# Kernel tuning notes

Hardware: AMD Instinct MI355X
Metric: run time of the kernel (lower is better)

The kernel has to match this reference:

```python
import jax, jax.numpy as jnp
import numpy as np

# GCN ('gcn' variant): avg-pooled adjacency, per-step linear + propagation + ReLU,
# final output projection, then select the target (first) node of each block.
# The original builds a dense block-diagonal (B*n, B*n) adjacency via torch.block_diag;
# since off-block entries are exactly zero, this is mathematically identical to
# batched per-block matmuls, which is what we do here.

B, N_NODES, D_IN, D_HID, D_OUT, STEPS = 256, 512, 256, 256, 128, 3


def setup_inputs() -> dict:
    key = jax.random.key(0)
    ks = jax.random.split(key, 6)
    xavier = lambda k, shp: jax.random.normal(k, shp, jnp.float32) * np.sqrt(2.0 / (shp[0] + shp[1]))
    feat = jax.random.normal(ks[0], (B * N_NODES, D_IN), jnp.float32)
    raw_adj = jax.random.uniform(ks[1], (B, N_NODES, N_NODES), jnp.float32)
    W0 = xavier(ks[2], (D_IN, D_HID))
    W1 = xavier(ks[3], (D_HID, D_HID))
    W2 = xavier(ks[4], (D_HID, D_HID))
    Wout = xavier(ks[5], (D_HID, D_OUT))
    return {"feat": feat, "raw_adj": raw_adj, "W0": W0, "W1": W1, "W2": W2, "Wout": Wout}


def reference(feat, raw_adj, W0, W1, W2, Wout):
    b, n, _ = raw_adj.shape
    d = feat.shape[1]
    Xb = feat.reshape(b, n, d)  # block view of feat

    # avg_pooling: row-normalize adjacency by the sum over columns whose
    # feature rows are nonzero (block-diagonal => per-block computation).
    nz = (jnp.linalg.norm(Xb, axis=2) > 0).astype(raw_adj.dtype)  # (b, n)
    row_sum = jnp.einsum('bij,bj->bi', raw_adj, nz)               # (b, n)
    row_sum = jnp.where(row_sum == 0, 1.0, row_sum)
    adj = raw_adj / row_sum[:, :, None]

    X = Xb
    for W in (W0, W1, W2):
        Z = jnp.einsum('bnd,dh->bnh', X, W)      # per-step linear (no bias)
        X = jax.nn.relu(jnp.einsum('bij,bjh->bih', adj, Z))  # propagate + ReLU
    out = jnp.einsum('bnh,ho->bno', X, Wout)     # output layer
    # X[ids] with ids = [0, n, 2n, ...] == first node of each block
    return out[:, 0, :]
```

## Files before the change

kernel.cpp:

```cpp
#include <hip/hip_runtime.h>


typedef __attribute__((ext_vector_type(8))) short short8;
typedef __attribute__((ext_vector_type(4))) float f32x4;

__device__ __forceinline__ unsigned short f2bf(float x) {
  unsigned u = __float_as_uint(x);
  unsigned r = u + 0x7fffu + ((u >> 16) & 1u);
  return (unsigned short)(r >> 16);
}
__device__ __forceinline__ float bf2f(unsigned short b) {
  return __uint_as_float(((unsigned)b) << 16);
}
__device__ __forceinline__ unsigned pkbf(float lo, float hi) {
  unsigned r;
  asm("v_cvt_pk_bf16_f32 %0, %1, %2" : "=v"(r) : "v"(lo), "v"(hi));
  return r;
}

#define GLDS(g, l) __builtin_amdgcn_global_load_lds( \
    (const __attribute__((address_space(1))) void*)(g), \
    (__attribute__((address_space(3))) void*)(l), 16, 0, 0)

__device__ __forceinline__ int swz2048(int bid) { return (bid & 7) * 256 + (bid >> 3); }

__global__ void k_wconv(const float* __restrict__ W0, const float* __restrict__ W1,
                        unsigned short* __restrict__ Wt) {
  int s = blockIdx.x >> 8;
  int n = blockIdx.x & 255;
  int k = threadIdx.x;
  const float* W = s ? W1 : W0;
  Wt[(size_t)s * 65536 + n * 256 + k] = f2bf(W[(size_t)k * 256 + n]);
}

__global__ void k_adj(const float* __restrict__ adj, const float* __restrict__ nz,
                      unsigned short* __restrict__ adjN) {
  int row = blockIdx.x * 4 + (threadIdx.x >> 6);
  int lane = threadIdx.x & 63;
  int b = row >> 9;
  const float4* src = (const float4*)(adj + (size_t)row * 512);
  float4 a0 = src[lane * 2], a1 = src[lane * 2 + 1];
  const float4* nzp = (const float4*)(nz + (size_t)b * 512);
  float4 z0 = nzp[lane * 2], z1 = nzp[lane * 2 + 1];
  float s = a0.x * z0.x + a0.y * z0.y + a0.z * z0.z + a0.w * z0.w
          + a1.x * z1.x + a1.y * z1.y + a1.z * z1.z + a1.w * z1.w;
#pragma unroll
  for (int off = 1; off < 64; off <<= 1) s += __shfl_xor(s, off);
  float inv = 1.f / ((s == 0.f) ? 1.f : s);
  uint4 p;
  p.x = pkbf(a0.x * inv, a0.y * inv);
  p.y = pkbf(a0.z * inv, a0.w * inv);
  p.z = pkbf(a1.x * inv, a1.y * inv);
  p.w = pkbf(a1.z * inv, a1.w * inv);
  ((uint4*)(adjN + (size_t)row * 512))[lane] = p;
}

__device__ __forceinline__ void gemm_tile(
    const char* Ag, int ldaB, const char* Bg, int ldbB, int nkt,
    char* ldsA, char* ldsB, f32x4 acc[4][4], int wm, int wn, int lane, int tid) {
  for (int kt = 0; kt < nkt; ++kt) {
#pragma unroll
    for (int q = 0; q < 4; ++q) {
      int P = (q * 256 + tid) * 16;
      int L = P ^ (((P >> 7) & 7) << 4);
      int row = L >> 7, cb = L & 127;
      GLDS(Ag + (size_t)row * ldaB + kt * 128 + cb, ldsA + P);
      GLDS(Bg + (size_t)row * ldbB + kt * 128 + cb, ldsB + P);
    }
    __syncthreads();
#pragma unroll
    for (int ks = 0; ks < 2; ++ks) {
      short8 af[4], bfr[4];
      int c = ks * 64 + ((lane >> 4) << 4);
#pragma unroll
      for (int m = 0; m < 4; ++m) {
        int row = wm * 64 + m * 16 + (lane & 15);
        af[m] = *(const short8*)(ldsA + ((row * 128 + c) ^ ((row & 7) << 4)));
      }
#pragma unroll
      for (int n = 0; n < 4; ++n) {
        int row = wn * 64 + n * 16 + (lane & 15);
        bfr[n] = *(const short8*)(ldsB + ((row * 128 + c) ^ ((row & 7) << 4)));
      }
#pragma unroll
      for (int m = 0; m < 4; ++m)
#pragma unroll
        for (int n = 0; n < 4; ++n)
          acc[m][n] = __builtin_amdgcn_mfma_f32_16x16x32_bf16(af[m], bfr[n], acc[m][n], 0, 0, 0);
    }
    __syncthreads();
  }
}

__global__ __launch_bounds__(256) void k_lin0(const float* __restrict__ feat,
                                              const unsigned short* __restrict__ Wt,
                                              unsigned short* __restrict__ Zt,
                                              float* __restrict__ nzOut) {
  __shared__ char ldsA[16384];
  __shared__ char ldsB[16384];
  int tid = threadIdx.x, lane = tid & 63, wid = tid >> 6;
  int wm = wid >> 1, wn = wid & 1;
  int tile = swz2048(blockIdx.x);
  int tm = tile >> 1, tn = tile & 1;
  const float* Ag = feat + (size_t)tm * 128 * 256;
  const char* Bg = (const char*)(Wt + (size_t)tn * 128 * 256);
  int r = tid >> 1, hk = tid & 1;
  const float* myrow = Ag + (size_t)r * 256 + hk * 32;
  float ssq = 0.f;
  f32x4 acc[4][4];
#pragma unroll
  for (int m = 0; m < 4; ++m)
#pragma unroll
    for (int n = 0; n < 4; ++n) { f32x4 z = {0.f, 0.f, 0.f, 0.f}; acc[m][n] = z; }

  for (int kt = 0; kt < 4; ++kt) {
#pragma unroll
    for (int q = 0; q < 4; ++q) {
      int P = (q * 256 + tid) * 16;
      int L = P ^ (((P >> 7) & 7) << 4);
      int row = L >> 7, cb = L & 127;
      GLDS(Bg + (size_t)row * 512 + kt * 128 + cb, ldsB + P);
    }
    float4 f[8];
#pragma unroll
    for (int q = 0; q < 8; ++q) f[q] = ((const float4*)(myrow + kt * 64))[q];
#pragma unroll
    for (int q = 0; q < 8; ++q)
      ssq += f[q].x * f[q].x + f[q].y * f[q].y + f[q].z * f[q].z + f[q].w * f[q].w;
#pragma unroll
    for (int q = 0; q < 4; ++q) {
      uint4 w;
      w.x = pkbf(f[2 * q].x, f[2 * q].y);
      w.y = pkbf(f[2 * q].z, f[2 * q].w);
      w.z = pkbf(f[2 * q + 1].x, f[2 * q + 1].y);
      w.w = pkbf(f[2 * q + 1].z, f[2 * q + 1].w);
      int cb = hk * 64 + q * 16;
      *(uint4*)(ldsA + ((r * 128 + cb) ^ ((r & 7) << 4))) = w;
    }
    __syncthreads();
#pragma unroll
    for (int ks = 0; ks < 2; ++ks) {
      short8 af[4], bfr[4];
      int c = ks * 64 + ((lane >> 4) << 4);
#pragma unroll
      for (int m = 0; m < 4; ++m) {
        int row = wm * 64 + m * 16 + (lane & 15);
        af[m] = *(const short8*)(ldsA + ((row * 128 + c) ^ ((row & 7) << 4)));
      }
#pragma unroll
      for (int n = 0; n < 4; ++n) {
        int row = wn * 64 + n * 16 + (lane & 15);
        bfr[n] = *(const short8*)(ldsB + ((row * 128 + c) ^ ((row & 7) << 4)));
      }
#pragma unroll
      for (int m = 0; m < 4; ++m)
#pragma unroll
        for (int n = 0; n < 4; ++n)
          acc[m][n] = __builtin_amdgcn_mfma_f32_16x16x32_bf16(af[m], bfr[n], acc[m][n], 0, 0, 0);
    }
    __syncthreads();
  }

  float tot = ssq + __shfl_xor(ssq, 1);
  if (hk == 0 && tn == 0) nzOut[(size_t)tm * 128 + r] = (tot > 0.f) ? 1.f : 0.f;

  int b = tm >> 2;
  int node_base = ((tm & 3) * 128) + wm * 64;
  int h_base = tn * 128 + wn * 64;
#pragma unroll
  for (int m = 0; m < 4; ++m) {
    int node = node_base + m * 16 + ((lane >> 4) << 2);
#pragma unroll
    for (int n = 0; n < 4; ++n) {
      int h = h_base + n * 16 + (lane & 15);
      f32x4 v = acc[m][n];
      ushort4 p;
      p.x = f2bf(v[0]); p.y = f2bf(v[1]); p.z = f2bf(v[2]); p.w = f2bf(v[3]);
      *(ushort4*)(Zt + ((size_t)b * 256 + h) * 512 + node) = p;
    }
  }
}

__global__ __launch_bounds__(256) void k_prop(const unsigned short* __restrict__ adjN,
                                              const unsigned short* __restrict__ Zt,
                                              unsigned short* __restrict__ Xout) {
  __shared__ char lds[32768];
  int tid = threadIdx.x, lane = tid & 63, wid = tid >> 6;
  int wm = wid >> 1, wn = wid & 1;
  int tile = swz2048(blockIdx.x);
  int b = tile >> 3, tm = (tile >> 1) & 3, tn = tile & 1;
  const char* Ag = (const char*)(adjN + ((size_t)b * 512 + tm * 128) * 512);
  const char* Bg = (const char*)(Zt + ((size_t)b * 256 + tn * 128) * 512);
  f32x4 acc[4][4];
#pragma unroll
  for (int m = 0; m < 4; ++m)
#pragma unroll
    for (int n = 0; n < 4; ++n) { f32x4 z = {0.f, 0.f, 0.f, 0.f}; acc[m][n] = z; }
  gemm_tile(Ag, 1024, Bg, 1024, 8, lds, lds + 16384, acc, wm, wn, lane, tid);
  int node_base = tm * 128 + wm * 64;
  int h_base = tn * 128 + wn * 64;
#pragma unroll
  for (int m = 0; m < 4; ++m) {
    int node = node_base + m * 16 + ((lane >> 4) << 2);
#pragma unroll
    for (int n = 0; n < 4; ++n) {
      int h = h_base + n * 16 + (lane & 15);
#pragma unroll
      for (int r = 0; r < 4; ++r) {
        float v = acc[m][n][r];
        v = v > 0.f ? v : 0.f;
        Xout[((size_t)b * 512 + node + r) * 256 + h] = f2bf(v);
      }
    }
  }
}

__global__ __launch_bounds__(256) void k_linear(const unsigned short* __restrict__ X,
                                                const unsigned short* __restrict__ Wt,
                                                unsigned short* __restrict__ Zt) {
  __shared__ char lds[32768];
  int tid = threadIdx.x, lane = tid & 63, wid = tid >> 6;
  int wm = wid >> 1, wn = wid & 1;
  int tile = swz2048(blockIdx.x);
  int tm = tile >> 1, tn = tile & 1;
  const char* Ag = (const char*)(X + (size_t)tm * 128 * 256);
  const char* Bg = (const char*)(Wt + (size_t)tn * 128 * 256);
  f32x4 acc[4][4];
#pragma unroll
  for (int m = 0; m < 4; ++m)
#pragma unroll
    for (int n = 0; n < 4; ++n) { f32x4 z = {0.f, 0.f, 0.f, 0.f}; acc[m][n] = z; }
  gemm_tile(Ag, 512, Bg, 512, 4, lds, lds + 16384, acc, wm, wn, lane, tid);
  int b = tm >> 2;
  int node_base = ((tm & 3) * 128) + wm * 64;
  int h_base = tn * 128 + wn * 64;
#pragma unroll
  for (int m = 0; m < 4; ++m) {
    int node = node_base + m * 16 + ((lane >> 4) << 2);
#pragma unroll
    for (int n = 0; n < 4; ++n) {
      int h = h_base + n * 16 + (lane & 15);
      f32x4 v = acc[m][n];
      ushort4 p;
      p.x = f2bf(v[0]); p.y = f2bf(v[1]); p.z = f2bf(v[2]); p.w = f2bf(v[3]);
      *(ushort4*)(Zt + ((size_t)b * 256 + h) * 512 + node) = p;
    }
  }
}

__global__ __launch_bounds__(256) void k_tail(const unsigned short* __restrict__ adjN,
                                              const unsigned short* __restrict__ X2,
                                              const float* __restrict__ W2,
                                              const float* __restrict__ Wout,
                                              float* __restrict__ out) {
  __shared__ float aL[512];
  __shared__ float yL[8][256];
  __shared__ float y[256];
  __shared__ float x3[256];
  int b = blockIdx.x, tid = threadIdx.x;
  {
    const unsigned short* a0 = adjN + (size_t)b * 512 * 512;
    ushort2 v = ((const ushort2*)a0)[tid];
    aL[tid * 2] = bf2f(v.x);
    aL[tid * 2 + 1] = bf2f(v.y);
  }
  __syncthreads();
  {
    int hg = tid & 31, jg = tid >> 5;
    float acc8[8] = {0.f, 0.f, 0.f, 0.f, 0.f, 0.f, 0.f, 0.f};
    const unsigned short* Xb = X2 + (size_t)b * 512 * 256;
    for (int jj = 0; jj < 64; ++jj) {
      int j = jj * 8 + jg;
      short8 xv = *(const short8*)(Xb + (size_t)j * 256 + hg * 8);
      float a = aL[j];
#pragma unroll
      for (int r = 0; r < 8; ++r) acc8[r] += a * bf2f((unsigned short)xv[r]);
    }
#pragma unroll
    for (int r = 0; r < 8; ++r) yL[jg][hg * 8 + r] = acc8[r];
  }
  __syncthreads();
  {
    float s = 0.f;
#pragma unroll
    for (int g = 0; g < 8; ++g) s += yL[g][tid];
    y[tid] = s;
  }
  __syncthreads();
  {
    float s = 0.f;
    for (int k = 0; k < 256; ++k) s += y[k] * W2[(size_t)k * 256 + tid];
    x3[tid] = s > 0.f ? s : 0.f;
  }
  __syncthreads();
  if (tid < 128) {
    float s = 0.f;
    for (int h = 0; h < 256; ++h) s += x3[h] * Wout[(size_t)h * 128 + tid];
    out[(size_t)b * 128 + tid] = s;
  }
}

extern "C" void kernel_launch(void* const* d_in, const int* in_sizes, int n_in,
                              void* d_out, int out_size, void* d_ws, size_t ws_size,
                              hipStream_t stream) {
  (void)in_sizes; (void)n_in; (void)out_size; (void)ws_size;
  const float* feat = (const float*)d_in[0];
  const float* adj  = (const float*)d_in[1];
  const float* W0   = (const float*)d_in[2];
  const float* W1   = (const float*)d_in[3];
  const float* W2   = (const float*)d_in[4];
  const float* Wout = (const float*)d_in[5];
  float* out = (float*)d_out;

  char* ws = (char*)d_ws;
  unsigned short* adjN = (unsigned short*)(ws);
  unsigned short* Xbuf = (unsigned short*)(ws + 134217728);
  unsigned short* Zt   = (unsigned short*)(ws + 201326592);
  float* nzbuf         = (float*)(ws + 268435456);
  unsigned short* Wt   = (unsigned short*)(ws + 268959744);

  k_wconv<<<512, 256, 0, stream>>>(W0, W1, Wt);
  k_lin0<<<2048, 256, 0, stream>>>(feat, Wt, Zt, nzbuf);
  k_adj<<<32768, 256, 0, stream>>>(adj, nzbuf, adjN);
  k_prop<<<2048, 256, 0, stream>>>(adjN, Zt, Xbuf);
  k_linear<<<2048, 256, 0, stream>>>(Xbuf, Wt + 65536, Zt);
  k_prop<<<2048, 256, 0, stream>>>(adjN, Zt, Xbuf);
  k_tail<<<256, 256, 0, stream>>>(adjN, Xbuf, W2, Wout, out);
}
```

Before: 342.2 us.

## Double-buffer GEMM LDS staging and fuse the last propagation with row-0 reduction

The shared GEMM tile loop now double-buffers its LDS stages, so the global-to-LDS loads for the next K tile are issued while MFMAs run on the current one. The second propagation kernel no longer writes the full X2 activation. It applies ReLU and immediately reduces against row 0 of the adjacency to produce partial y vectors, which the tail kernel then sums. This removes a full X2 write and re-read plus the tail's gather pass. In exchange, LDS per block doubles to 64KB, which may lower occupancy.

```diff
diff --git a/kernel.cpp b/kernel.cpp
--- a/kernel.cpp
+++ b/kernel.cpp
@@ -55,19 +55,27 @@
   ((uint4*)(adjN + (size_t)row * 512))[lane] = p;
 }
 
-__device__ __forceinline__ void gemm_tile(
+__device__ __forceinline__ void gemm_dbuf(
     const char* Ag, int ldaB, const char* Bg, int ldbB, int nkt,
-    char* ldsA, char* ldsB, f32x4 acc[4][4], int wm, int wn, int lane, int tid) {
+    char* lds, f32x4 acc[4][4], int wm, int wn, int lane, int tid) {
+  char* ldsA = lds;
+  char* ldsB = lds + 32768;
+#define STAGE_AB(KT, BUF) do {                                           \
+    _Pragma("unroll")                                                    \
+    for (int q = 0; q < 4; ++q) {                                        \
+      int P = (q * 256 + tid) * 16;                                      \
+      int L = P ^ (((P >> 7) & 7) << 4);                                 \
+      int row = L >> 7, cb = L & 127;                                    \
+      GLDS(Ag + (size_t)row * ldaB + (KT) * 128 + cb,                    \
+           ldsA + (BUF) * 16384 + P);                                    \
+      GLDS(Bg + (size_t)row * ldbB + (KT) * 128 + cb,                    \
+           ldsB + (BUF) * 16384 + P);                                    \
+    } } while (0)
+  STAGE_AB(0, 0);
+  __syncthreads();
   for (int kt = 0; kt < nkt; ++kt) {
-#pragma unroll
-    for (int q = 0; q < 4; ++q) {
-      int P = (q * 256 + tid) * 16;
-      int L = P ^ (((P >> 7) & 7) << 4);
-      int row = L >> 7, cb = L & 127;
-      GLDS(Ag + (size_t)row * ldaB + kt * 128 + cb, ldsA + P);
-      GLDS(Bg + (size_t)row * ldbB + kt * 128 + cb, ldsB + P);
-    }
-    __syncthreads();
+    int cur = kt & 1;
+    if (kt + 1 < nkt) STAGE_AB(kt + 1, cur ^ 1);
 #pragma unroll
     for (int ks = 0; ks < 2; ++ks) {
       short8 af[4], bfr[4];
@@ -75,12 +83,12 @@
 #pragma unroll
       for (int m = 0; m < 4; ++m) {
         int row = wm * 64 + m * 16 + (lane & 15);
-        af[m] = *(const short8*)(ldsA + ((row * 128 + c) ^ ((row & 7) << 4)));
+        af[m] = *(const short8*)(ldsA + cur * 16384 + ((row * 128 + c) ^ ((row & 7) << 4)));
       }
 #pragma unroll
       for (int n = 0; n < 4; ++n) {
         int row = wn * 64 + n * 16 + (lane & 15);
-        bfr[n] = *(const short8*)(ldsB + ((row * 128 + c) ^ ((row & 7) << 4)));
+        bfr[n] = *(const short8*)(ldsB + cur * 16384 + ((row * 128 + c) ^ ((row & 7) << 4)));
       }
 #pragma unroll
       for (int m = 0; m < 4; ++m)
@@ -90,6 +98,7 @@
     }
     __syncthreads();
   }
+#undef STAGE_AB
 }
 
 __global__ __launch_bounds__(256) void k_lin0(const float* __restrict__ feat,
@@ -184,7 +193,7 @@
 __global__ __launch_bounds__(256) void k_prop(const unsigned short* __restrict__ adjN,
                                               const unsigned short* __restrict__ Zt,
                                               unsigned short* __restrict__ Xout) {
-  __shared__ char lds[32768];
+  __shared__ char lds[65536];
   int tid = threadIdx.x, lane = tid & 63, wid = tid >> 6;
   int wm = wid >> 1, wn = wid & 1;
   int tile = swz2048(blockIdx.x);
@@ -196,7 +205,7 @@
   for (int m = 0; m < 4; ++m)
 #pragma unroll
     for (int n = 0; n < 4; ++n) { f32x4 z = {0.f, 0.f, 0.f, 0.f}; acc[m][n] = z; }
-  gemm_tile(Ag, 1024, Bg, 1024, 8, lds, lds + 16384, acc, wm, wn, lane, tid);
+  gemm_dbuf(Ag, 1024, Bg, 1024, 8, lds, acc, wm, wn, lane, tid);
   int node_base = tm * 128 + wm * 64;
   int h_base = tn * 128 + wn * 64;
 #pragma unroll
@@ -215,10 +224,58 @@
   }
 }
 
+__global__ __launch_bounds__(256) void k_propy(const unsigned short* __restrict__ adjN,
+                                               const unsigned short* __restrict__ Zt,
+                                               float* __restrict__ yws) {
+  __shared__ char lds[65536];
+  __shared__ float ybuf[2][128];
+  int tid = threadIdx.x, lane = tid & 63, wid = tid >> 6;
+  int wm = wid >> 1, wn = wid & 1;
+  int tile = swz2048(blockIdx.x);
+  int b = tile >> 3, tm = (tile >> 1) & 3, tn = tile & 1;
+  const char* Ag = (const char*)(adjN + ((size_t)b * 512 + tm * 128) * 512);
+  const char* Bg = (const char*)(Zt + ((size_t)b * 256 + tn * 128) * 512);
+  f32x4 acc[4][4];
+#pragma unroll
+  for (int m = 0; m < 4; ++m)
+#pragma unroll
+    for (int n = 0; n < 4; ++n) { f32x4 z = {0.f, 0.f, 0.f, 0.f}; acc[m][n] = z; }
+  gemm_dbuf(Ag, 1024, Bg, 1024, 8, lds, acc, wm, wn, lane, tid);
+
+  int kq = lane >> 4, r0 = lane & 15;
+  float yp[4] = {0.f, 0.f, 0.f, 0.f};
+#pragma unroll
+  for (int m = 0; m < 4; ++m) {
+    int node = tm * 128 + wm * 64 + m * 16 + kq * 4;
+    ushort4 a4 = *(const ushort4*)(adjN + (size_t)b * 262144 + node);
+    float a[4] = {bf2f(a4.x), bf2f(a4.y), bf2f(a4.z), bf2f(a4.w)};
+#pragma unroll
+    for (int n = 0; n < 4; ++n)
+#pragma unroll
+      for (int r = 0; r < 4; ++r) {
+        float v = acc[m][n][r];
+        v = v > 0.f ? v : 0.f;
+        yp[n] += v * a[r];
+      }
+  }
+#pragma unroll
+  for (int n = 0; n < 4; ++n) {
+    yp[n] += __shfl_xor(yp[n], 16);
+    yp[n] += __shfl_xor(yp[n], 32);
+  }
+  if (lane < 16) {
+#pragma unroll
+    for (int n = 0; n < 4; ++n) ybuf[wm][wn * 64 + n * 16 + lane] = yp[n];
+  }
+  __syncthreads();
+  if (tid < 128)
+    yws[((size_t)b * 4 + tm) * 256 + tn * 128 + tid] = ybuf[0][tid] + ybuf[1][tid];
+}
+
 __global__ __launch_bounds__(256) void k_linear(const unsigned short* __restrict__ X,
                                                 const unsigned short* __restrict__ Wt,
                                                 unsigned short* __restrict__ Zt) {
-  __shared__ char lds[32768];
+  __shared__ char lds[65536];
   int tid = threadIdx.x, lane = tid & 63, wid = tid >> 6;
   int wm = wid >> 1, wn = wid & 1;
   int tile = swz2048(blockIdx.x);
@@ -230,7 +287,7 @@
   for (int m = 0; m < 4; ++m)
 #pragma unroll
     for (int n = 0; n < 4; ++n) { f32x4 z = {0.f, 0.f, 0.f, 0.f}; acc[m][n] = z; }
-  gemm_tile(Ag, 512, Bg, 512, 4, lds, lds + 16384, acc, wm, wn, lane, tid);
+  gemm_dbuf(Ag, 512, Bg, 512, 4, lds, acc, wm, wn, lane, tid);
   int b = tm >> 2;
   int node_base = ((tm & 3) * 128) + wm * 64;
   int h_base = tn * 128 + wn * 64;
@@ -248,44 +305,15 @@
   }
 }
 
-__global__ __launch_bounds__(256) void k_tail(const unsigned short* __restrict__ adjN,
-                                              const unsigned short* __restrict__ X2,
+__global__ __launch_bounds__(256) void k_tail(const float* __restrict__ yws,
                                               const float* __restrict__ W2,
                                               const float* __restrict__ Wout,
                                               float* __restrict__ out) {
-  __shared__ float aL[512];
-  __shared__ float yL[8][256];
   __shared__ float y[256];
   __shared__ float x3[256];
   int b = blockIdx.x, tid = threadIdx.x;
-  {
-    const unsigned short* a0 = adjN + (size_t)b * 512 * 512;
-    ushort2 v = ((const ushort2*)a0)[tid];
-    aL[tid * 2] = bf2f(v.x);
-    aL[tid * 2 + 1] = bf2f(v.y);
-  }
-  __syncthreads();
-  {
-    int hg = tid & 31, jg = tid >> 5;
-    float acc8[8] = {0.f, 0.f, 0.f, 0.f, 0.f, 0.f, 0.f, 0.f};
-    const unsigned short* Xb = X2 + (size_t)b * 512 * 256;
-    for (int jj = 0; jj < 64; ++jj) {
-      int j = jj * 8 + jg;
-      short8 xv = *(const short8*)(Xb + (size_t)j * 256 + hg * 8);
-      float a = aL[j];
-#pragma unroll
-      for (int r = 0; r < 8; ++r) acc8[r] += a * bf2f((unsigned short)xv[r]);
-    }
-#pragma unroll
-    for (int r = 0; r < 8; ++r) yL[jg][hg * 8 + r] = acc8[r];
-  }
-  __syncthreads();
-  {
-    float s = 0.f;
-#pragma unroll
-    for (int g = 0; g < 8; ++g) s += yL[g][tid];
-    y[tid] = s;
-  }
+  const float* w = yws + (size_t)b * 1024;
+  y[tid] = w[tid] + w[256 + tid] + w[512 + tid] + w[768 + tid];
   __syncthreads();
   {
     float s = 0.f;
@@ -318,12 +346,13 @@
   unsigned short* Zt   = (unsigned short*)(ws + 201326592);
   float* nzbuf         = (float*)(ws + 268435456);
   unsigned short* Wt   = (unsigned short*)(ws + 268959744);
+  float* yws           = (float*)(ws + 269221888);
 
   k_wconv<<<512, 256, 0, stream>>>(W0, W1, Wt);
   k_lin0<<<2048, 256, 0, stream>>>(feat, Wt, Zt, nzbuf);
   k_adj<<<32768, 256, 0, stream>>>(adj, nzbuf, adjN);
   k_prop<<<2048, 256, 0, stream>>>(adjN, Zt, Xbuf);
   k_linear<<<2048, 256, 0, stream>>>(Xbuf, Wt + 65536, Zt);
-  k_prop<<<2048, 256, 0, stream>>>(adjN, Zt, Xbuf);
-  k_tail<<<256, 256, 0, stream>>>(adjN, Xbuf, W2, Wout, out);
-}
+  k_propy<<<2048, 256, 0, stream>>>(adjN, Zt, yws);
+  k_tail<<<256, 256, 0, stream>>>(yws, W2, Wout, out);
+}
```

After: 315.0 us. 1.09x faster.
